# Performance work log

Hardware: AMD Instinct MI355X
Metric: run time of the kernel (lower is better)

## Reference

```python
import jax, jax.numpy as jnp
import numpy as np
import math

B = 512
EMB = 512
CLASSNUM = 70722
M = 0.4
H = 0.333
S = 64.0
EPS = 1e-3


def setup_inputs() -> dict:
    key = jax.random.key(0)
    k1, k2, k3, k4, k5 = jax.random.split(key, 5)
    embbedings = jax.random.normal(k1, (B, EMB), dtype=jnp.float32)
    # feature norms: positive, realistic range ~[1, 30)
    norms = jax.random.uniform(k2, (B, 1), dtype=jnp.float32) * 29.0 + 1.0
    label = jax.random.randint(k3, (B,), 0, CLASSNUM, dtype=jnp.int64)
    class_sample_num_ = jax.random.uniform(k4, (B,), dtype=jnp.float32) * 9.0 + 1.0
    kernel = jax.random.normal(k5, (EMB, CLASSNUM), dtype=jnp.float32)
    return {
        "embbedings": embbedings,
        "norms": norms,
        "label": label,
        "class_sample_num_": class_sample_num_,
        "kernel": kernel,
    }


def reference(embbedings, norms, label, class_sample_num_, kernel):
    # l2-normalize kernel columns (axis=0)
    kernel_norm = kernel / jnp.linalg.norm(kernel, axis=0, keepdims=True)
    cosine = jnp.matmul(embbedings, kernel_norm)  # [B, C]
    cosine = jnp.clip(cosine, -1.0 + EPS, 1.0 - EPS)

    # detached margin scaler path (torch uses .detach / no_grad)
    safe_norms = jnp.clip(norms, 0.001, 100.0)
    safe_norms = safe_norms / (class_sample_num_[:, None] + 0.001)
    safe_norms = jnp.clip(safe_norms, 0.001, 100.0)
    safe_norms = jax.lax.stop_gradient(safe_norms)

    mean = jnp.mean(safe_norms)
    std = jnp.std(safe_norms, ddof=1)  # torch.std is unbiased
    # t_alpha = 1.0 => batch stats are exactly this batch's mean/std
    batch_mean, batch_std = mean, std

    margin_scaler = (safe_norms - batch_mean) / (batch_std + EPS)
    margin_scaler = jnp.clip(margin_scaler * H, -1.0, 1.0)  # [B, 1]
    ms = margin_scaler[:, 0]  # [B]

    rows = jnp.arange(B)
    lab = label.astype(jnp.int32)

    # angular margin: theta_m = clip(theta + onehot * (-m*ms))
    theta = jnp.arccos(cosine)
    theta = theta.at[rows, lab].add(-M * ms)
    theta_m = jnp.clip(theta, EPS, math.pi - EPS)
    cosine2 = jnp.cos(theta_m)

    # additive margin at the label column: g_add = m + m*ms
    cosine2 = cosine2.at[rows, lab].add(-(M + M * ms))

    return cosine2 * S
```

## Files before the change

kernel.cpp:

```cpp
#include <hip/hip_runtime.h>
#include <math.h>

#define CLASSNUM 70722
#define BATCH 512
#define EMBD 512
#define M_C 0.4f
#define H_C 0.333f
#define S_C 64.0f
#define EPS_C 0.001f
#define PI_F 3.14159265358979f

typedef __bf16 bf16_t;
typedef __bf16 bf16x4 __attribute__((ext_vector_type(4)));
typedef __bf16 bf16x8 __attribute__((ext_vector_type(8)));
typedef float f32x4 __attribute__((ext_vector_type(4)));

__device__ __forceinline__ float clampf(float x, float lo, float hi) {
    return fminf(fmaxf(x, lo), hi);
}

__global__ __launch_bounds__(256) void prep_lab_kernel(
    const float* __restrict__ emb, const float* __restrict__ norms,
    const float* __restrict__ csn, const int* __restrict__ label,
    const float* __restrict__ kmat, bf16_t* __restrict__ Aws,
    float* __restrict__ labout)
{
    __shared__ float red[256];
    const int tid = threadIdx.x;
    const int bi = blockIdx.x;

    if (bi < 128) {
        const int G = bi * 256 + tid;
        const int kt = G >> 11;
        const int rem = G & 2047;
        const int rg = rem >> 6;
        const int lane = rem & 63;
        const int row = rg * 16 + (lane & 15);
        const int k0 = kt * 32 + (lane >> 4) * 8;
        const float* src = emb + row * EMBD + k0;
        const float4 v0 = *(const float4*)src;
        const float4 v1 = *(const float4*)(src + 4);
        bf16x8 bw;
        bw[0] = (bf16_t)v0.x; bw[1] = (bf16_t)v0.y;
        bw[2] = (bf16_t)v0.z; bw[3] = (bf16_t)v0.w;
        bw[4] = (bf16_t)v1.x; bw[5] = (bf16_t)v1.y;
        bw[6] = (bf16_t)v1.z; bw[7] = (bf16_t)v1.w;
        *(bf16x8*)(Aws + (size_t)G * 8) = bw;
        return;
    }

    const int b = bi - 128;

    float s0, s1;
    {
        float sn = clampf(norms[tid], 0.001f, 100.0f);
        sn = sn / (csn[tid] + 0.001f);
        s0 = clampf(sn, 0.001f, 100.0f);
    }
    {
        float sn = clampf(norms[tid + 256], 0.001f, 100.0f);
        sn = sn / (csn[tid + 256] + 0.001f);
        s1 = clampf(sn, 0.001f, 100.0f);
    }
    red[tid] = s0 + s1;
    __syncthreads();
    for (int off = 128; off > 0; off >>= 1) {
        if (tid < off) red[tid] += red[tid + off];
        __syncthreads();
    }
    const float mean = red[0] * (1.0f / 512.0f);
    __syncthreads();
    const float d0 = s0 - mean, d1 = s1 - mean;
    red[tid] = d0 * d0 + d1 * d1;
    __syncthreads();
    for (int off = 128; off > 0; off >>= 1) {
        if (tid < off) red[tid] += red[tid + off];
        __syncthreads();
    }
    const float stdv = sqrtf(red[0] * (1.0f / 511.0f));
    __syncthreads();

    const int lab = label[b];
    const float* col = kmat + lab;
    const float* e = emb + b * EMBD;
    float dot = 0.0f, ss = 0.0f;
#pragma unroll
    for (int k = tid; k < EMBD; k += 256) {
        const float kv = col[(size_t)k * CLASSNUM];
        const float ev = e[k];
        dot = fmaf(ev, kv, dot);
        ss  = fmaf(kv, kv, ss);
    }
    red[tid] = dot;
    __syncthreads();
    for (int off = 128; off > 0; off >>= 1) {
        if (tid < off) red[tid] += red[tid + off];
        __syncthreads();
    }
    const float dotT = red[0];
    __syncthreads();
    red[tid] = ss;
    __syncthreads();
    for (int off = 128; off > 0; off >>= 1) {
        if (tid < off) red[tid] += red[tid + off];
        __syncthreads();
    }
    if (tid == 0) {
        const float ssT = red[0];
        float c = dotT / sqrtf(ssT);
        c = clampf(c, -1.0f + EPS_C, 1.0f - EPS_C);
        float snb = clampf(norms[b], 0.001f, 100.0f);
        snb = snb / (csn[b] + 0.001f);
        snb = clampf(snb, 0.001f, 100.0f);
        const float msv = clampf((snb - mean) / (stdv + EPS_C) * H_C, -1.0f, 1.0f);
        float th = acosf(c) - M_C * msv;
        th = clampf(th, EPS_C, PI_F - EPS_C);
        labout[b] = (cosf(th) - (M_C + M_C * msv)) * S_C;
    }
}


#define LOADB4(t, dst) do {                                             \
    const size_t ko_ = (size_t)((t) * 32) * CLASSNUM;                   \
    _Pragma("unroll")                                                   \
    for (int j_ = 0; j_ < 4; ++j_)                                      \
        dst[j_] = bp[ko_ + (size_t)j_ * CLASSNUM];                      \
} while (0)

#define LOADA4(t, af) do {                                              \
    const bf16x8* ap_ = (const bf16x8*)Aws                              \
        + (((t) * 32 + wave * 4) * 64 + lane);                          \
    _Pragma("unroll")                                                   \
    for (int mi_ = 0; mi_ < 4; ++mi_) af[mi_] = ap_[mi_ * 64];          \
} while (0)

#define CVTW(src, buf) do {                                             \
    bf16x4 w_;                                                          \
    _Pragma("unroll")                                                   \
    for (int j_ = 0; j_ < 4; ++j_) {                                    \
        const float v_ = src[j_];                                       \
        ssq = fmaf(v_, v_, ssq);                                        \
        w_[j_] = (bf16_t)v_;                                            \
    }                                                                   \
    *(bf16x4*)&Blds[buf][c * 40 + kg * 4] = w_;                         \
} while (0)

#define MFMA16(af, buf) do {                                            \
    bf16x8 bfr_[4];                                                     \
    _Pragma("unroll")                                                   \
    for (int ni_ = 0; ni_ < 4; ++ni_)                                   \
        bfr_[ni_] = *(const bf16x8*)                                    \
            &Blds[buf][(ni_ * 16 + r16) * 40 + quad * 8];               \
    _Pragma("unroll")                                                   \
    for (int mi_ = 0; mi_ < 4; ++mi_)                                   \
        _Pragma("unroll")                                               \
        for (int ni_ = 0; ni_ < 4; ++ni_)                               \
            acc[mi_][ni_] = __builtin_amdgcn_mfma_f32_16x16x32_bf16(    \
                af[mi_], bfr_[ni_], acc[mi_][ni_], 0, 0, 0);            \
} while (0)

#define BARRIER() do {                                                  \
    asm volatile("s_waitcnt lgkmcnt(0)" ::: "memory");                  \
    __builtin_amdgcn_s_barrier();                                       \
} while (0)

__global__ __launch_bounds__(512, 4) void gemm_kernel(
    const bf16_t* __restrict__ Aws, const float* __restrict__ Kmat,
    const int* __restrict__ label, const float* __restrict__ labout,
    float* __restrict__ out)
{
    __shared__ bf16_t Blds[2][64 * 40];
    __shared__ float red[512];
    __shared__ float invn_s[64];
    __shared__ int   lab_s[BATCH];
    __shared__ float lo_s[BATCH];

    const int tid  = threadIdx.x;
    const int lane = tid & 63;
    const int wave = tid >> 6;
    const int r16  = lane & 15;
    const int quad = lane >> 4;

    const int nwg = (CLASSNUM + 63) / 64;
    const int q_ = nwg >> 3, r_ = nwg & 7;
    const int xcd = blockIdx.x & 7, idx = blockIdx.x >> 3;
    const int nb = (xcd < r_) ? (xcd * (q_ + 1) + idx)
                              : (r_ * (q_ + 1) + (xcd - r_) * q_ + idx);
    const int n0 = nb * 64;

    lab_s[tid] = label[tid];
    lo_s[tid]  = labout[tid];

    const int c  = tid & 63;
    const int kg = tid >> 6;
    int cg = n0 + c;
    const bool cv = (cg < CLASSNUM);
    if (!cv) cg = CLASSNUM - 1;
    const float* bp = Kmat + (size_t)(kg * 4) * CLASSNUM + cg;

    f32x4 acc[4][4];
    const f32x4 zero = {0.0f, 0.0f, 0.0f, 0.0f};
#pragma unroll
    for (int i = 0; i < 4; ++i)
#pragma unroll
        for (int j = 0; j < 4; ++j) acc[i][j] = zero;
    float ssq = 0.0f;

    float bv0[4], bv1[4];

    LOADB4(0, bv0);
    LOADB4(1, bv1);
    CVTW(bv0, 0);
    BARRIER();

#pragma unroll 1
    for (int p = 0; p < 8; ++p) {
        {
            bf16x8 af[4];
            LOADA4(2 * p, af);
            if (p < 7) LOADB4(2 * p + 2, bv0);
            MFMA16(af, 0);
            CVTW(bv1, 1);
            BARRIER();
        }
        {
            bf16x8 af[4];
            LOADA4(2 * p + 1, af);
            if (p < 7) LOADB4(2 * p + 3, bv1);
            MFMA16(af, 1);
            if (p < 7) CVTW(bv0, 0);
            BARRIER();
        }
    }

    red[tid] = ssq;
    __syncthreads();
    if (tid < 64) {
        float s = 0.0f;
#pragma unroll
        for (int g = 0; g < 8; ++g) s += red[tid + g * 64];
        invn_s[tid] = (s > 0.0f) ? (1.0f / sqrtf(s)) : 0.0f;
    }
    __syncthreads();

#pragma unroll
    for (int mi = 0; mi < 4; ++mi) {
#pragma unroll
        for (int rr = 0; rr < 4; ++rr) {
            const int row = wave * 64 + mi * 16 + quad * 4 + rr;
            const int labc = lab_s[row];
            const float lov = lo_s[row];
            float* orow = out + (size_t)row * CLASSNUM;
#pragma unroll
            for (int ni = 0; ni < 4; ++ni) {
                const int col_loc = ni * 16 + r16;
                const int col = n0 + col_loc;
                if (col < CLASSNUM) {
                    const float cc = clampf(acc[mi][ni][rr] * invn_s[col_loc],
                                            -1.0f + EPS_C, 1.0f - EPS_C);
                    float v = cc * S_C;
                    if (labc == col) v = lov;
                    orow[col] = v;
                }
            }
        }
    }
}

extern "C" void kernel_launch(void* const* d_in, const int* in_sizes, int n_in,
                              void* d_out, int out_size, void* d_ws, size_t ws_size,
                              hipStream_t stream)
{
    const float* emb   = (const float*)d_in[0];
    const float* norms = (const float*)d_in[1];
    const int*   label = (const int*)d_in[2];
    const float* csn   = (const float*)d_in[3];
    const float* kmat  = (const float*)d_in[4];
    float* out = (float*)d_out;

    const size_t A_BYTES = (size_t)BATCH * EMBD * sizeof(bf16_t);
    if (ws_size < A_BYTES + 4096) return;
    bf16_t* Aws   = (bf16_t*)d_ws;
    float* labout = (float*)((char*)d_ws + A_BYTES);

    prep_lab_kernel<<<128 + BATCH, 256, 0, stream>>>(
        emb, norms, csn, label, kmat, Aws, labout);
    const int nblk = (CLASSNUM + 63) / 64;
    gemm_kernel<<<nblk, 512, 0, stream>>>(Aws, kmat, label, labout, out);
}
```

Measured before the change: 317.0 us.

## Split GEMM workgroups across batch halves with 256 threads and 8-wide B loads

Each GEMM workgroup now handles 256 of the 512 batch rows with 4 waves instead of 8. Twice as many blocks are launched, and paired halves sit adjacently in the XCD swizzle. Each thread loads and converts 8 k-values of the kernel matrix per step instead of 4. MFMA sections are wrapped with s_setprio to favour matrix issue. The aim is more blocks in flight and smaller workgroups, at the cost of reading the kernel matrix and recomputing its column norms twice.

```diff
diff --git a/kernel.cpp b/kernel.cpp
--- a/kernel.cpp
+++ b/kernel.cpp
@@ -11,7 +11,6 @@
 #define PI_F 3.14159265358979f
 
 typedef __bf16 bf16_t;
-typedef __bf16 bf16x4 __attribute__((ext_vector_type(4)));
 typedef __bf16 bf16x8 __attribute__((ext_vector_type(8)));
 typedef float f32x4 __attribute__((ext_vector_type(4)));
 
@@ -120,29 +119,29 @@
 }
 
 
-#define LOADB4(t, dst) do {                                             \
+#define LOADB8(t, dst) do {                                             \
     const size_t ko_ = (size_t)((t) * 32) * CLASSNUM;                   \
     _Pragma("unroll")                                                   \
-    for (int j_ = 0; j_ < 4; ++j_)                                      \
+    for (int j_ = 0; j_ < 8; ++j_)                                      \
         dst[j_] = bp[ko_ + (size_t)j_ * CLASSNUM];                      \
 } while (0)
 
 #define LOADA4(t, af) do {                                              \
     const bf16x8* ap_ = (const bf16x8*)Aws                              \
-        + (((t) * 32 + wave * 4) * 64 + lane);                          \
+        + (((t) * 32 + mbase + wave * 4) * 64 + lane);                  \
     _Pragma("unroll")                                                   \
     for (int mi_ = 0; mi_ < 4; ++mi_) af[mi_] = ap_[mi_ * 64];          \
 } while (0)
 
-#define CVTW(src, buf) do {                                             \
-    bf16x4 w_;                                                          \
-    _Pragma("unroll")                                                   \
-    for (int j_ = 0; j_ < 4; ++j_) {                                    \
+#define CVTW8(src, buf) do {                                            \
+    bf16x8 w_;                                                          \
+    _Pragma("unroll")                                                   \
+    for (int j_ = 0; j_ < 8; ++j_) {                                    \
         const float v_ = src[j_];                                       \
         ssq = fmaf(v_, v_, ssq);                                        \
         w_[j_] = (bf16_t)v_;                                            \
     }                                                                   \
-    *(bf16x4*)&Blds[buf][c * 40 + kg * 4] = w_;                         \
+    *(bf16x8*)&Blds[buf][c * 40 + kg * 8] = w_;                         \
 } while (0)
 
 #define MFMA16(af, buf) do {                                            \
@@ -151,12 +150,14 @@
     for (int ni_ = 0; ni_ < 4; ++ni_)                                   \
         bfr_[ni_] = *(const bf16x8*)                                    \
             &Blds[buf][(ni_ * 16 + r16) * 40 + quad * 8];               \
+    __builtin_amdgcn_s_setprio(1);                                      \
     _Pragma("unroll")                                                   \
     for (int mi_ = 0; mi_ < 4; ++mi_)                                   \
         _Pragma("unroll")                                               \
         for (int ni_ = 0; ni_ < 4; ++ni_)                               \
             acc[mi_][ni_] = __builtin_amdgcn_mfma_f32_16x16x32_bf16(    \
                 af[mi_], bfr_[ni_], acc[mi_][ni_], 0, 0, 0);            \
+    __builtin_amdgcn_s_setprio(0);                                      \
 } while (0)
 
 #define BARRIER() do {                                                  \
@@ -164,16 +165,16 @@
     __builtin_amdgcn_s_barrier();                                       \
 } while (0)
 
-__global__ __launch_bounds__(512, 4) void gemm_kernel(
+__global__ __launch_bounds__(256, 4) void gemm_kernel(
     const bf16_t* __restrict__ Aws, const float* __restrict__ Kmat,
     const int* __restrict__ label, const float* __restrict__ labout,
     float* __restrict__ out)
 {
     __shared__ bf16_t Blds[2][64 * 40];
-    __shared__ float red[512];
+    __shared__ float red[256];
     __shared__ float invn_s[64];
-    __shared__ int   lab_s[BATCH];
-    __shared__ float lo_s[BATCH];
+    __shared__ int   lab_s[256];
+    __shared__ float lo_s[256];
 
     const int tid  = threadIdx.x;
     const int lane = tid & 63;
@@ -181,22 +182,23 @@
     const int r16  = lane & 15;
     const int quad = lane >> 4;
 
-    const int nwg = (CLASSNUM + 63) / 64;
+    const int nwg = 2 * ((CLASSNUM + 63) / 64);
     const int q_ = nwg >> 3, r_ = nwg & 7;
     const int xcd = blockIdx.x & 7, idx = blockIdx.x >> 3;
-    const int nb = (xcd < r_) ? (xcd * (q_ + 1) + idx)
-                              : (r_ * (q_ + 1) + (xcd - r_) * q_ + idx);
-    const int n0 = nb * 64;
-
-    lab_s[tid] = label[tid];
-    lo_s[tid]  = labout[tid];
+    const int swz = (xcd < r_) ? (xcd * (q_ + 1) + idx)
+                               : (r_ * (q_ + 1) + (xcd - r_) * q_ + idx);
+    const int mhalf = swz & 1;
+    const int n0    = (swz >> 1) * 64;
+    const int mbase = mhalf * 16;
+
+    lab_s[tid] = label[mhalf * 256 + tid];
+    lo_s[tid]  = labout[mhalf * 256 + tid];
 
     const int c  = tid & 63;
     const int kg = tid >> 6;
     int cg = n0 + c;
-    const bool cv = (cg < CLASSNUM);
-    if (!cv) cg = CLASSNUM - 1;
-    const float* bp = Kmat + (size_t)(kg * 4) * CLASSNUM + cg;
+    if (cg >= CLASSNUM) cg = CLASSNUM - 1;
+    const float* bp = Kmat + (size_t)(kg * 8) * CLASSNUM + cg;
 
     f32x4 acc[4][4];
     const f32x4 zero = {0.0f, 0.0f, 0.0f, 0.0f};
@@ -206,11 +208,11 @@
         for (int j = 0; j < 4; ++j) acc[i][j] = zero;
     float ssq = 0.0f;
 
-    float bv0[4], bv1[4];
-
-    LOADB4(0, bv0);
-    LOADB4(1, bv1);
-    CVTW(bv0, 0);
+    float bv0[8], bv1[8];
+
+    LOADB8(0, bv0);
+    LOADB8(1, bv1);
+    CVTW8(bv0, 0);
     BARRIER();
 
 #pragma unroll 1
@@ -218,17 +220,17 @@
         {
             bf16x8 af[4];
             LOADA4(2 * p, af);
-            if (p < 7) LOADB4(2 * p + 2, bv0);
+            if (p < 7) LOADB8(2 * p + 2, bv0);
             MFMA16(af, 0);
-            CVTW(bv1, 1);
+            CVTW8(bv1, 1);
             BARRIER();
         }
         {
             bf16x8 af[4];
             LOADA4(2 * p + 1, af);
-            if (p < 7) LOADB4(2 * p + 3, bv1);
+            if (p < 7) LOADB8(2 * p + 3, bv1);
             MFMA16(af, 1);
-            if (p < 7) CVTW(bv0, 0);
+            if (p < 7) CVTW8(bv0, 0);
             BARRIER();
         }
     }
@@ -236,9 +238,7 @@
     red[tid] = ssq;
     __syncthreads();
     if (tid < 64) {
-        float s = 0.0f;
-#pragma unroll
-        for (int g = 0; g < 8; ++g) s += red[tid + g * 64];
+        const float s = red[tid] + red[tid + 64] + red[tid + 128] + red[tid + 192];
         invn_s[tid] = (s > 0.0f) ? (1.0f / sqrtf(s)) : 0.0f;
     }
     __syncthreads();
@@ -247,10 +247,10 @@
     for (int mi = 0; mi < 4; ++mi) {
 #pragma unroll
         for (int rr = 0; rr < 4; ++rr) {
-            const int row = wave * 64 + mi * 16 + quad * 4 + rr;
-            const int labc = lab_s[row];
-            const float lov = lo_s[row];
-            float* orow = out + (size_t)row * CLASSNUM;
+            const int rowl = wave * 64 + mi * 16 + quad * 4 + rr;
+            const int labc = lab_s[rowl];
+            const float lov = lo_s[rowl];
+            float* orow = out + (size_t)(mhalf * 256 + rowl) * CLASSNUM;
 #pragma unroll
             for (int ni = 0; ni < 4; ++ni) {
                 const int col_loc = ni * 16 + r16;
@@ -285,6 +285,6 @@
 
     prep_lab_kernel<<<128 + BATCH, 256, 0, stream>>>(
         emb, norms, csn, label, kmat, Aws, labout);
-    const int nblk = (CLASSNUM + 63) / 64;
-    gemm_kernel<<<nblk, 512, 0, stream>>>(Aws, kmat, label, labout, out);
-}
+    const int nblk = 2 * ((CLASSNUM + 63) / 64);
+    gemm_kernel<<<nblk, 256, 0, stream>>>(Aws, kmat, label, labout, out);
+}
```

After: 333.6 us. 5.2% more time.
